# Kernel tuning notes

Hardware: AMD Instinct MI355X
Metric: run time of the kernel (lower is better)

Reference implementation:

```python
import jax, jax.numpy as jnp
import numpy as np

B, T = 64, 50  # batch, decode steps (max_sequence_length)


def setup_inputs() -> dict:
    key = jax.random.key(0)
    ks = jax.random.split(key, 6)
    D, H, V = 512, 1024, 32000
    s = 0.02
    return {
        "sequence_embedding": jax.random.normal(ks[0], (B, H), jnp.float32),
        "emb_table": jax.random.normal(ks[1], (V, D), jnp.float32) * s,
        "W_ih": jax.random.normal(ks[2], (3 * H, D), jnp.float32) * s,
        "W_hh": jax.random.normal(ks[3], (3 * H, H), jnp.float32) * s,
        "b_ih": jnp.zeros((3 * H,), jnp.float32),
        "b_hh": jnp.zeros((3 * H,), jnp.float32),
        "fc_w": jax.random.normal(ks[4], (V, H), jnp.float32) * s,
        "fc_b": jnp.zeros((V,), jnp.float32),
        "eos_index": 0,
    }


def _gru_cell(x, h, W_ih, W_hh, b_ih, b_hh):
    # Standard GRU cell (torch GRUCell math). x: [B, D], h: [B, H]
    gi = x @ W_ih.T + b_ih            # [B, 3H]
    gh = h @ W_hh.T + b_hh            # [B, 3H]
    i_r, i_z, i_n = jnp.split(gi, 3, axis=-1)
    h_r, h_z, h_n = jnp.split(gh, 3, axis=-1)
    r = jax.nn.sigmoid(i_r + h_r)
    z = jax.nn.sigmoid(i_z + h_z)
    n = jnp.tanh(i_n + r * h_n)
    return (1.0 - z) * n + z * h


def reference(sequence_embedding, emb_table, W_ih, W_hh, b_ih, b_hh, fc_w, fc_b, eos_index):
    # Initial input: EOS token embedding broadcast over batch. [B, D]
    x0 = jnp.broadcast_to(emb_table[eos_index], (B, emb_table.shape[1]))
    h0 = sequence_embedding  # num_layers=1: initial hidden = sequence embedding
    keys = jax.random.split(jax.random.key(42), T)

    def step(carry, k):
        x, h = carry
        h = _gru_cell(x, h, W_ih, W_hh, b_ih, b_hh)
        logits = h @ fc_w.T + fc_b              # [B, V]
        idx = jax.random.categorical(k, logits)  # multinomial sample, [B]
        x = emb_table[idx]                       # next-step input embedding
        return (x, h), (idx, logits)

    (_, _), (indices, logits) = jax.lax.scan(step, (x0, h0), keys)
    return indices, logits  # [T, B] int, [T, B, V] float
```

## Files before the change

### kernel.cpp

```cpp
#include <hip/hip_runtime.h>
#include <stdint.h>

#define BB 64
#define DD 512
#define HH 1024
#define VV 32000
#define T_STEPS 50
#define G3 3072
#define NBLK_LOG (VV / 64)

typedef __attribute__((ext_vector_type(8))) short bf16x8;
typedef __attribute__((ext_vector_type(4))) float f32x4;
typedef unsigned long long u64;
typedef unsigned short ushort_t;

__device__ __forceinline__ uint32_t rotl32(uint32_t x, int d) {
  return (x << d) | (x >> (32 - d));
}

__device__ __forceinline__ void threefry2x32(uint32_t k0, uint32_t k1,
                                             uint32_t& x0, uint32_t& x1) {
  uint32_t ks0 = k0, ks1 = k1, ks2 = k0 ^ k1 ^ 0x1BD11BDAu;
  x0 += ks0; x1 += ks1;
#define TF_R(r) { x0 += x1; x1 = rotl32(x1, (r)); x1 ^= x0; }
  TF_R(13) TF_R(15) TF_R(26) TF_R(6)
  x0 += ks1; x1 += ks2 + 1u;
  TF_R(17) TF_R(29) TF_R(16) TF_R(24)
  x0 += ks2; x1 += ks0 + 2u;
  TF_R(13) TF_R(15) TF_R(26) TF_R(6)
  x0 += ks0; x1 += ks1 + 3u;
  TF_R(17) TF_R(29) TF_R(16) TF_R(24)
  x0 += ks1; x1 += ks2 + 4u;
  TF_R(13) TF_R(15) TF_R(26) TF_R(6)
  x0 += ks2; x1 += ks0 + 5u;
#undef TF_R
}

__device__ __forceinline__ uint32_t f2bf(float f) {
  uint32_t u = __float_as_uint(f);
  return (u + 0x7fffu + ((u >> 16) & 1u)) >> 16;
}
__device__ __forceinline__ float bf2f(uint32_t b) { return __uint_as_float(b << 16); }

__device__ __forceinline__ u64 packkey(float v, int c) {
  uint32_t s = __float_as_uint(v);
  uint32_t mo = (s & 0x80000000u) ? ~s : (s | 0x80000000u);
  return ((u64)mo << 32) | (uint32_t)(~(uint32_t)c);
}
__device__ __forceinline__ u64 umax64(u64 a, u64 b) { return a > b ? a : b; }

template<int EPI>
__device__ __forceinline__ void mfma_body(
    ushort_t (*__restrict__ bhS)[40], ushort_t (*__restrict__ blS)[40],
    u64 (*__restrict__ scr)[2],
    const ushort_t* __restrict__ Ahi, const ushort_t* __restrict__ Alo,
    const float* __restrict__ Bw, int K,
    const float* __restrict__ bias,
    float* __restrict__ C, int ldc, int n0,
    u64* __restrict__ partial, int nblk, int bid, int t)
{
  const int tid = threadIdx.x;
  const int lane = tid & 63, w = tid >> 6;
  const int l15 = lane & 15, q = lane >> 4;
  const int rw = (w >> 1) * 32, cw = (w & 1) * 32;

  f32x4 acc[2][2] = {};

  const int srow = tid >> 2;
  const int schunk = (tid & 3) * 8;

  for (int k0 = 0; k0 < K; k0 += 32) {
    const float* bp = Bw + (size_t)(n0 + srow) * K + k0 + schunk;
    float4 v0 = *(const float4*)bp;
    float4 v1 = *(const float4*)(bp + 4);

    bf16x8 ah[2], al[2];
#pragma unroll
    for (int m = 0; m < 2; ++m) {
      const size_t ao = (size_t)(rw + 16 * m + l15) * K + k0 + 8 * q;
      ah[m] = *(const bf16x8*)(Ahi + ao);
      al[m] = *(const bf16x8*)(Alo + ao);
    }

    __syncthreads();
    {
      float f[8] = {v0.x, v0.y, v0.z, v0.w, v1.x, v1.y, v1.z, v1.w};
      uint32_t ph[4], pl[4];
#pragma unroll
      for (int i = 0; i < 4; ++i) {
        float a = f[2 * i], b = f[2 * i + 1];
        uint32_t ha = f2bf(a), hb = f2bf(b);
        float ra = a - bf2f(ha), rb = b - bf2f(hb);
        ph[i] = ha | (hb << 16);
        pl[i] = f2bf(ra) | (f2bf(rb) << 16);
      }
      *(uint4*)&bhS[srow][schunk] = make_uint4(ph[0], ph[1], ph[2], ph[3]);
      *(uint4*)&blS[srow][schunk] = make_uint4(pl[0], pl[1], pl[2], pl[3]);
    }
    __syncthreads();

    bf16x8 bhf[2], blf[2];
#pragma unroll
    for (int n = 0; n < 2; ++n) {
      bhf[n] = *(const bf16x8*)&bhS[cw + 16 * n + l15][8 * q];
      blf[n] = *(const bf16x8*)&blS[cw + 16 * n + l15][8 * q];
    }
#pragma unroll
    for (int m = 0; m < 2; ++m)
#pragma unroll
      for (int n = 0; n < 2; ++n) {
        acc[m][n] = __builtin_amdgcn_mfma_f32_16x16x32_bf16(ah[m], bhf[n], acc[m][n], 0, 0, 0);
        acc[m][n] = __builtin_amdgcn_mfma_f32_16x16x32_bf16(ah[m], blf[n], acc[m][n], 0, 0, 0);
        acc[m][n] = __builtin_amdgcn_mfma_f32_16x16x32_bf16(al[m], bhf[n], acc[m][n], 0, 0, 0);
      }
  }

  if constexpr (EPI == 0) {
#pragma unroll
    for (int m = 0; m < 2; ++m)
#pragma unroll
      for (int n = 0; n < 2; ++n)
#pragma unroll
        for (int r = 0; r < 4; ++r) {
          int row = rw + 16 * m + 4 * q + r;
          int col = n0 + cw + 16 * n + l15;
          C[(size_t)row * ldc + col] = acc[m][n][r];
        }
  } else {
    uint32_t kt0 = 0u, kt1 = (uint32_t)t;
    threefry2x32(0u, 42u, kt0, kt1);

    u64 bk[2][4];
#pragma unroll
    for (int m = 0; m < 2; ++m)
#pragma unroll
      for (int r = 0; r < 4; ++r) bk[m][r] = 0ull;

#pragma unroll
    for (int m = 0; m < 2; ++m)
#pragma unroll
      for (int n = 0; n < 2; ++n)
#pragma unroll
        for (int r = 0; r < 4; ++r) {
          int row = rw + 16 * m + 4 * q + r;
          int col = n0 + cw + 16 * n + l15;
          float val = acc[m][n][r] + bias[col];
          C[(size_t)row * ldc + col] = val;
          uint32_t c0 = 0u, c1 = (uint32_t)(row * VV + col);
          threefry2x32(kt0, kt1, c0, c1);
          uint32_t bits = c0 ^ c1;
          float u = __uint_as_float((bits >> 9) | 0x3f800000u) - 1.0f;
          if (u == 0.0f) u = 1.17549435e-38f;
          float g = -__logf(-__logf(u));
          bk[m][r] = umax64(bk[m][r], packkey(val + g, col));
        }
#pragma unroll
    for (int off = 1; off < 16; off <<= 1)
#pragma unroll
      for (int m = 0; m < 2; ++m)
#pragma unroll
        for (int r = 0; r < 4; ++r)
          bk[m][r] = umax64(bk[m][r], (u64)__shfl_xor((long long)bk[m][r], off, 64));

    if (l15 == 0) {
#pragma unroll
      for (int m = 0; m < 2; ++m)
#pragma unroll
        for (int r = 0; r < 4; ++r)
          scr[rw + 16 * m + 4 * q + r][w & 1] = bk[m][r];
    }
    __syncthreads();
    if (tid < 64) {
      u64 fk = umax64(scr[tid][0], scr[tid][1]);
      partial[(size_t)tid * nblk + bid] = fk;
    }
  }
}

__global__ __launch_bounds__(256) void gates_mfma(
    const ushort_t* __restrict__ xh, const ushort_t* __restrict__ xl,
    const float* __restrict__ Wih,
    const ushort_t* __restrict__ hh, const ushort_t* __restrict__ hl,
    const float* __restrict__ Whh,
    float* __restrict__ gi, float* __restrict__ gh)
{
  __shared__ ushort_t bhS[64][40];
  __shared__ ushort_t blS[64][40];
  __shared__ u64 scr[64][2];
  if (blockIdx.x < G3 / 64)
    mfma_body<0>(bhS, blS, scr, xh, xl, Wih, DD, nullptr, gi, G3,
                 blockIdx.x * 64, nullptr, 0, 0, 0);
  else
    mfma_body<0>(bhS, blS, scr, hh, hl, Whh, HH, nullptr, gh, G3,
                 (blockIdx.x - G3 / 64) * 64, nullptr, 0, 0, 0);
}

__global__ __launch_bounds__(256) void logits_mfma(
    const ushort_t* __restrict__ hh, const ushort_t* __restrict__ hl,
    const float* __restrict__ fcw, const float* __restrict__ fcb,
    float* __restrict__ lg, u64* __restrict__ partial, int t)
{
  __shared__ ushort_t bhS[64][40];
  __shared__ ushort_t blS[64][40];
  __shared__ u64 scr[64][2];
  mfma_body<1>(bhS, blS, scr, hh, hl, fcw, HH, fcb, lg, VV,
               blockIdx.x * 64, partial, NBLK_LOG, blockIdx.x, t);
}

__global__ __launch_bounds__(256) void gru_gate(
    const float* __restrict__ gi, const float* __restrict__ gh,
    const float* __restrict__ bih, const float* __restrict__ bhh,
    float* __restrict__ h, ushort_t* __restrict__ hhi, ushort_t* __restrict__ hlo)
{
  int i = blockIdx.x * 256 + threadIdx.x;
  int b = i >> 10, j = i & 1023;
  const float* gib = gi + (size_t)b * G3;
  const float* ghb = gh + (size_t)b * G3;
  float ir = gib[j]        + bih[j],        hr = ghb[j]        + bhh[j];
  float iz = gib[j + 1024] + bih[j + 1024], hz = ghb[j + 1024] + bhh[j + 1024];
  float in_ = gib[j + 2048] + bih[j + 2048], hn = ghb[j + 2048] + bhh[j + 2048];
  float r = 1.f / (1.f + expf(-(ir + hr)));
  float z = 1.f / (1.f + expf(-(iz + hz)));
  float n = tanhf(in_ + r * hn);
  float hv = (1.f - z) * n + z * h[i];
  h[i] = hv;
  uint32_t hb = f2bf(hv);
  hhi[i] = (ushort_t)hb;
  hlo[i] = (ushort_t)f2bf(hv - bf2f(hb));
}

__global__ __launch_bounds__(256) void finish_sample(
    const u64* __restrict__ partial, const float* __restrict__ emb,
    float* __restrict__ idx_out, ushort_t* __restrict__ xh, ushort_t* __restrict__ xl)
{
  __shared__ u64 red[256];
  __shared__ int sidx;
  const int b = blockIdx.x, tid = threadIdx.x;
  u64 best = 0;
  for (int i = tid; i < NBLK_LOG; i += 256) {
    u64 v = partial[(size_t)b * NBLK_LOG + i];
    if (v > best) best = v;
  }
  red[tid] = best;
  __syncthreads();
  for (int s = 128; s > 0; s >>= 1) {
    if (tid < s) { if (red[tid + s] > red[tid]) red[tid] = red[tid + s]; }
    __syncthreads();
  }
  if (tid == 0) {
    int idx = (int)(~(uint32_t)red[0]);
    sidx = idx;
    idx_out[b] = (float)idx;
  }
  __syncthreads();
  const float2* ep = (const float2*)(emb + (size_t)sidx * DD);
  float2 v = ep[tid];
  uint32_t h0 = f2bf(v.x), h1 = f2bf(v.y);
  uint32_t l0 = f2bf(v.x - bf2f(h0)), l1 = f2bf(v.y - bf2f(h1));
  *(uint32_t*)&xh[(size_t)b * DD + 2 * tid] = h0 | (h1 << 16);
  *(uint32_t*)&xl[(size_t)b * DD + 2 * tid] = l0 | (l1 << 16);
}

__global__ __launch_bounds__(256) void init_kernel(
    const float* __restrict__ seq, const float* __restrict__ emb,
    const int* __restrict__ eos, float* __restrict__ h,
    ushort_t* __restrict__ hhi, ushort_t* __restrict__ hlo,
    ushort_t* __restrict__ xh, ushort_t* __restrict__ xl)
{
  int i = blockIdx.x * 256 + threadIdx.x;
  if (i < BB * HH) {
    float v = seq[i];
    h[i] = v;
    uint32_t hb = f2bf(v);
    hhi[i] = (ushort_t)hb;
    hlo[i] = (ushort_t)f2bf(v - bf2f(hb));
  }
  if (i < BB * DD) {
    float v = emb[(size_t)eos[0] * DD + (i & (DD - 1))];
    uint32_t hb = f2bf(v);
    xh[i] = (ushort_t)hb;
    xl[i] = (ushort_t)f2bf(v - bf2f(hb));
  }
}

extern "C" void kernel_launch(void* const* d_in, const int* in_sizes, int n_in,
                              void* d_out, int out_size, void* d_ws, size_t ws_size,
                              hipStream_t stream) {
  const float* seq = (const float*)d_in[0];
  const float* emb = (const float*)d_in[1];
  const float* Wih = (const float*)d_in[2];
  const float* Whh = (const float*)d_in[3];
  const float* bih = (const float*)d_in[4];
  const float* bhh = (const float*)d_in[5];
  const float* fcw = (const float*)d_in[6];
  const float* fcb = (const float*)d_in[7];
  const int*   eos = (const int*)d_in[8];

  float* out = (float*)d_out;
  float* idx_out = out;
  float* log_out = out + (size_t)T_STEPS * BB;

  uint8_t* wsp = (uint8_t*)d_ws;
  auto alloc = [&](size_t bytes) {
    uint8_t* p = wsp;
    wsp += (bytes + 255) & ~(size_t)255;
    return p;
  };
  float*    h    = (float*)alloc((size_t)BB * HH * 4);
  float*    gi   = (float*)alloc((size_t)BB * G3 * 4);
  float*    gh   = (float*)alloc((size_t)BB * G3 * 4);
  ushort_t* hhi  = (ushort_t*)alloc((size_t)BB * HH * 2);
  ushort_t* hlo  = (ushort_t*)alloc((size_t)BB * HH * 2);
  ushort_t* xh   = (ushort_t*)alloc((size_t)BB * DD * 2);
  ushort_t* xl   = (ushort_t*)alloc((size_t)BB * DD * 2);
  u64*      part = (u64*)alloc((size_t)BB * NBLK_LOG * 8);

  init_kernel<<<256, 256, 0, stream>>>(seq, emb, eos, h, hhi, hlo, xh, xl);

  for (int t = 0; t < T_STEPS; ++t) {
    float* lg = log_out + (size_t)t * BB * VV;
    gates_mfma<<<96, 256, 0, stream>>>(xh, xl, Wih, hhi, hlo, Whh, gi, gh);
    gru_gate<<<(BB * HH) / 256, 256, 0, stream>>>(gi, gh, bih, bhh, h, hhi, hlo);
    logits_mfma<<<NBLK_LOG, 256, 0, stream>>>(hhi, hlo, fcw, fcb, lg, part, t);
    finish_sample<<<BB, 256, 0, stream>>>(part, emb, idx_out + t * BB, xh, xl);
  }
}
```

Baseline: 3.830 ms.

## Fuse decoder into persistent cooperative kernel with precomputed embedding-input projections

After: 8.579 ms. 124% more time.

```diff
diff --git a/kernel.cpp b/kernel.cpp
--- a/kernel.cpp
+++ b/kernel.cpp
@@ -1,5 +1,8 @@
 #include <hip/hip_runtime.h>
+#include <hip/hip_cooperative_groups.h>
 #include <stdint.h>
+
+namespace cg = cooperative_groups;
 
 #define BB 64
 #define DD 512
@@ -7,7 +10,9 @@
 #define VV 32000
 #define T_STEPS 50
 #define G3 3072
-#define NBLK_LOG (VV / 64)
+#define NT 250
+#define GHT 24
+#define UT 12000
 
 typedef __attribute__((ext_vector_type(8))) short bf16x8;
 typedef __attribute__((ext_vector_type(4))) float f32x4;
@@ -49,25 +54,34 @@
 }
 __device__ __forceinline__ u64 umax64(u64 a, u64 b) { return a > b ? a : b; }
 
-template<int EPI>
-__device__ __forceinline__ void mfma_body(
+union BF8 { uint32_t u[4]; bf16x8 v; };
+
+__device__ __forceinline__ void split8(const float* f, bf16x8& hi, bf16x8& lo) {
+  BF8 H, L;
+#pragma unroll
+  for (int i = 0; i < 4; ++i) {
+    float a = f[2 * i], b = f[2 * i + 1];
+    uint32_t ha = f2bf(a), hb = f2bf(b);
+    float ra = a - bf2f(ha), rb = b - bf2f(hb);
+    H.u[i] = ha | (hb << 16);
+    L.u[i] = f2bf(ra) | (f2bf(rb) << 16);
+  }
+  hi = H.v; lo = L.v;
+}
+
+template<bool AF32>
+__device__ __forceinline__ void mfma_tile512(
     ushort_t (*__restrict__ bhS)[40], ushort_t (*__restrict__ blS)[40],
-    u64 (*__restrict__ scr)[2],
     const ushort_t* __restrict__ Ahi, const ushort_t* __restrict__ Alo,
-    const float* __restrict__ Bw, int K,
-    const float* __restrict__ bias,
-    float* __restrict__ C, int ldc, int n0,
-    u64* __restrict__ partial, int nblk, int bid, int t)
+    const float* __restrict__ Af, int lda,
+    const float* __restrict__ Bw, int K, int n0,
+    f32x4 acc[2][2])
 {
   const int tid = threadIdx.x;
   const int lane = tid & 63, w = tid >> 6;
   const int l15 = lane & 15, q = lane >> 4;
-  const int rw = (w >> 1) * 32, cw = (w & 1) * 32;
-
-  f32x4 acc[2][2] = {};
-
-  const int srow = tid >> 2;
-  const int schunk = (tid & 3) * 8;
+  const int rw = (w >> 2) * 32, cw = (w & 3) * 32;
+  const int srow = tid >> 2, schunk = (tid & 3) * 8;
 
   for (int k0 = 0; k0 < K; k0 += 32) {
     const float* bp = Bw + (size_t)(n0 + srow) * K + k0 + schunk;
@@ -77,25 +91,26 @@
     bf16x8 ah[2], al[2];
 #pragma unroll
     for (int m = 0; m < 2; ++m) {
-      const size_t ao = (size_t)(rw + 16 * m + l15) * K + k0 + 8 * q;
-      ah[m] = *(const bf16x8*)(Ahi + ao);
-      al[m] = *(const bf16x8*)(Alo + ao);
+      if constexpr (AF32) {
+        const float* ap = Af + (size_t)(rw + 16 * m + l15) * lda + k0 + 8 * q;
+        float4 a0 = *(const float4*)ap;
+        float4 a1 = *(const float4*)(ap + 4);
+        float f[8] = {a0.x, a0.y, a0.z, a0.w, a1.x, a1.y, a1.z, a1.w};
+        split8(f, ah[m], al[m]);
+      } else {
+        const size_t ao = (size_t)(rw + 16 * m + l15) * lda + k0 + 8 * q;
+        ah[m] = *(const bf16x8*)(Ahi + ao);
+        al[m] = *(const bf16x8*)(Alo + ao);
+      }
     }
 
     __syncthreads();
     {
       float f[8] = {v0.x, v0.y, v0.z, v0.w, v1.x, v1.y, v1.z, v1.w};
-      uint32_t ph[4], pl[4];
-#pragma unroll
-      for (int i = 0; i < 4; ++i) {
-        float a = f[2 * i], b = f[2 * i + 1];
-        uint32_t ha = f2bf(a), hb = f2bf(b);
-        float ra = a - bf2f(ha), rb = b - bf2f(hb);
-        ph[i] = ha | (hb << 16);
-        pl[i] = f2bf(ra) | (f2bf(rb) << 16);
-      }
-      *(uint4*)&bhS[srow][schunk] = make_uint4(ph[0], ph[1], ph[2], ph[3]);
-      *(uint4*)&blS[srow][schunk] = make_uint4(pl[0], pl[1], pl[2], pl[3]);
+      bf16x8 bh, bl;
+      split8(f, bh, bl);
+      *(bf16x8*)&bhS[srow][schunk] = bh;
+      *(bf16x8*)&blS[srow][schunk] = bl;
     }
     __syncthreads();
 
@@ -114,111 +129,108 @@
         acc[m][n] = __builtin_amdgcn_mfma_f32_16x16x32_bf16(al[m], bhf[n], acc[m][n], 0, 0, 0);
       }
   }
-
-  if constexpr (EPI == 0) {
+}
+
+__device__ __forceinline__ void store_tile512(f32x4 acc[2][2], float* __restrict__ C,
+                                              int ldc, int n0)
+{
+  const int tid = threadIdx.x, lane = tid & 63, w = tid >> 6;
+  const int l15 = lane & 15, q = lane >> 4;
+  const int rw = (w >> 2) * 32, cw = (w & 3) * 32;
+#pragma unroll
+  for (int m = 0; m < 2; ++m)
+#pragma unroll
+    for (int n = 0; n < 2; ++n)
+#pragma unroll
+      for (int r = 0; r < 4; ++r)
+        C[(size_t)(rw + 16 * m + 4 * q + r) * ldc + n0 + cw + 16 * n + l15] = acc[m][n][r];
+}
+
+__device__ __forceinline__ void sample_epi512(
+    f32x4 acc[2][2], u64 (*__restrict__ scr)[4],
+    const float* __restrict__ bias, float* __restrict__ C, int n0,
+    u64* __restrict__ partial, int jobid, int t)
+{
+  const int tid = threadIdx.x, lane = tid & 63, w = tid >> 6;
+  const int l15 = lane & 15, q = lane >> 4;
+  const int rw = (w >> 2) * 32, cw = (w & 3) * 32;
+
+  uint32_t kt0 = 0u, kt1 = (uint32_t)t;
+  threefry2x32(0u, 42u, kt0, kt1);
+
+  u64 bk[2][4];
+#pragma unroll
+  for (int m = 0; m < 2; ++m)
+#pragma unroll
+    for (int r = 0; r < 4; ++r) bk[m][r] = 0ull;
+
+#pragma unroll
+  for (int m = 0; m < 2; ++m)
+#pragma unroll
+    for (int n = 0; n < 2; ++n)
+#pragma unroll
+      for (int r = 0; r < 4; ++r) {
+        int row = rw + 16 * m + 4 * q + r;
+        int col = n0 + cw + 16 * n + l15;
+        float val = acc[m][n][r] + bias[col];
+        C[(size_t)row * VV + col] = val;
+        uint32_t c0 = 0u, c1 = (uint32_t)(row * VV + col);
+        threefry2x32(kt0, kt1, c0, c1);
+        uint32_t bits = c0 ^ c1;
+        float u = __uint_as_float((bits >> 9) | 0x3f800000u) - 1.0f;
+        if (u == 0.0f) u = 1.17549435e-38f;
+        float g = -__logf(-__logf(u));
+        bk[m][r] = umax64(bk[m][r], packkey(val + g, col));
+      }
+#pragma unroll
+  for (int off = 1; off < 16; off <<= 1)
 #pragma unroll
     for (int m = 0; m < 2; ++m)
 #pragma unroll
-      for (int n = 0; n < 2; ++n)
-#pragma unroll
-        for (int r = 0; r < 4; ++r) {
-          int row = rw + 16 * m + 4 * q + r;
-          int col = n0 + cw + 16 * n + l15;
-          C[(size_t)row * ldc + col] = acc[m][n][r];
-        }
-  } else {
-    uint32_t kt0 = 0u, kt1 = (uint32_t)t;
-    threefry2x32(0u, 42u, kt0, kt1);
-
-    u64 bk[2][4];
+      for (int r = 0; r < 4; ++r)
+        bk[m][r] = umax64(bk[m][r], (u64)__shfl_xor((long long)bk[m][r], off, 64));
+
+  if (l15 == 0) {
 #pragma unroll
     for (int m = 0; m < 2; ++m)
 #pragma unroll
-      for (int r = 0; r < 4; ++r) bk[m][r] = 0ull;
-
-#pragma unroll
-    for (int m = 0; m < 2; ++m)
-#pragma unroll
-      for (int n = 0; n < 2; ++n)
-#pragma unroll
-        for (int r = 0; r < 4; ++r) {
-          int row = rw + 16 * m + 4 * q + r;
-          int col = n0 + cw + 16 * n + l15;
-          float val = acc[m][n][r] + bias[col];
-          C[(size_t)row * ldc + col] = val;
-          uint32_t c0 = 0u, c1 = (uint32_t)(row * VV + col);
-          threefry2x32(kt0, kt1, c0, c1);
-          uint32_t bits = c0 ^ c1;
-          float u = __uint_as_float((bits >> 9) | 0x3f800000u) - 1.0f;
-          if (u == 0.0f) u = 1.17549435e-38f;
-          float g = -__logf(-__logf(u));
-          bk[m][r] = umax64(bk[m][r], packkey(val + g, col));
-        }
-#pragma unroll
-    for (int off = 1; off < 16; off <<= 1)
-#pragma unroll
-      for (int m = 0; m < 2; ++m)
-#pragma unroll
-        for (int r = 0; r < 4; ++r)
-          bk[m][r] = umax64(bk[m][r], (u64)__shfl_xor((long long)bk[m][r], off, 64));
-
-    if (l15 == 0) {
-#pragma unroll
-      for (int m = 0; m < 2; ++m)
-#pragma unroll
-        for (int r = 0; r < 4; ++r)
-          scr[rw + 16 * m + 4 * q + r][w & 1] = bk[m][r];
-    }
+      for (int r = 0; r < 4; ++r)
+        scr[rw + 16 * m + 4 * q + r][w & 3] = bk[m][r];
+  }
+  __syncthreads();
+  if (tid < 64) {
+    u64 f = umax64(umax64(scr[tid][0], scr[tid][1]),
+                   umax64(scr[tid][2], scr[tid][3]));
+    partial[(size_t)tid * NT + jobid] = f;
+  }
+  __syncthreads();
+}
+
+__device__ __forceinline__ int finish_reduce(const u64* __restrict__ partial,
+                                             int b, u64* __restrict__ sred)
+{
+  const int tid = threadIdx.x;
+  u64 best = 0;
+  if (tid < NT) best = partial[(size_t)b * NT + tid];
+  sred[tid] = best;
+  __syncthreads();
+  for (int s = 256; s > 0; s >>= 1) {
+    if (tid < s) sred[tid] = umax64(sred[tid], sred[tid + s]);
     __syncthreads();
-    if (tid < 64) {
-      u64 fk = umax64(scr[tid][0], scr[tid][1]);
-      partial[(size_t)tid * nblk + bid] = fk;
-    }
-  }
-}
-
-__global__ __launch_bounds__(256) void gates_mfma(
-    const ushort_t* __restrict__ xh, const ushort_t* __restrict__ xl,
-    const float* __restrict__ Wih,
-    const ushort_t* __restrict__ hh, const ushort_t* __restrict__ hl,
-    const float* __restrict__ Whh,
-    float* __restrict__ gi, float* __restrict__ gh)
-{
-  __shared__ ushort_t bhS[64][40];
-  __shared__ ushort_t blS[64][40];
-  __shared__ u64 scr[64][2];
-  if (blockIdx.x < G3 / 64)
-    mfma_body<0>(bhS, blS, scr, xh, xl, Wih, DD, nullptr, gi, G3,
-                 blockIdx.x * 64, nullptr, 0, 0, 0);
-  else
-    mfma_body<0>(bhS, blS, scr, hh, hl, Whh, HH, nullptr, gh, G3,
-                 (blockIdx.x - G3 / 64) * 64, nullptr, 0, 0, 0);
-}
-
-__global__ __launch_bounds__(256) void logits_mfma(
-    const ushort_t* __restrict__ hh, const ushort_t* __restrict__ hl,
-    const float* __restrict__ fcw, const float* __restrict__ fcb,
-    float* __restrict__ lg, u64* __restrict__ partial, int t)
-{
-  __shared__ ushort_t bhS[64][40];
-  __shared__ ushort_t blS[64][40];
-  __shared__ u64 scr[64][2];
-  mfma_body<1>(bhS, blS, scr, hh, hl, fcw, HH, fcb, lg, VV,
-               blockIdx.x * 64, partial, NBLK_LOG, blockIdx.x, t);
-}
-
-__global__ __launch_bounds__(256) void gru_gate(
-    const float* __restrict__ gi, const float* __restrict__ gh,
+  }
+  return (int)(~(uint32_t)sred[0]);
+}
+
+__device__ __forceinline__ void fuse_elem(
+    const float* __restrict__ gir, const float* __restrict__ ghr,
     const float* __restrict__ bih, const float* __restrict__ bhh,
-    float* __restrict__ h, ushort_t* __restrict__ hhi, ushort_t* __restrict__ hlo)
-{
-  int i = blockIdx.x * 256 + threadIdx.x;
-  int b = i >> 10, j = i & 1023;
-  const float* gib = gi + (size_t)b * G3;
-  const float* ghb = gh + (size_t)b * G3;
-  float ir = gib[j]        + bih[j],        hr = ghb[j]        + bhh[j];
-  float iz = gib[j + 1024] + bih[j + 1024], hz = ghb[j + 1024] + bhh[j + 1024];
-  float in_ = gib[j + 2048] + bih[j + 2048], hn = ghb[j + 2048] + bhh[j + 2048];
+    float* __restrict__ h, ushort_t* __restrict__ hhi, ushort_t* __restrict__ hlo,
+    int b, int j)
+{
+  int i = b * HH + j;
+  float ir  = gir[j]        + bih[j],        hr = ghr[j]        + bhh[j];
+  float iz  = gir[j + 1024] + bih[j + 1024], hz = ghr[j + 1024] + bhh[j + 1024];
+  float in_ = gir[j + 2048] + bih[j + 2048], hn = ghr[j + 2048] + bhh[j + 2048];
   float r = 1.f / (1.f + expf(-(ir + hr)));
   float z = 1.f / (1.f + expf(-(iz + hz)));
   float n = tanhf(in_ + r * hn);
@@ -229,58 +241,204 @@
   hlo[i] = (ushort_t)f2bf(hv - bf2f(hb));
 }
 
-__global__ __launch_bounds__(256) void finish_sample(
-    const u64* __restrict__ partial, const float* __restrict__ emb,
-    float* __restrict__ idx_out, ushort_t* __restrict__ xh, ushort_t* __restrict__ xl)
-{
-  __shared__ u64 red[256];
-  __shared__ int sidx;
-  const int b = blockIdx.x, tid = threadIdx.x;
-  u64 best = 0;
-  for (int i = tid; i < NBLK_LOG; i += 256) {
-    u64 v = partial[(size_t)b * NBLK_LOG + i];
-    if (v > best) best = v;
-  }
-  red[tid] = best;
-  __syncthreads();
-  for (int s = 128; s > 0; s >>= 1) {
-    if (tid < s) { if (red[tid + s] > red[tid]) red[tid] = red[tid + s]; }
-    __syncthreads();
-  }
-  if (tid == 0) {
-    int idx = (int)(~(uint32_t)red[0]);
-    sidx = idx;
-    idx_out[b] = (float)idx;
-  }
-  __syncthreads();
-  const float2* ep = (const float2*)(emb + (size_t)sidx * DD);
-  float2 v = ep[tid];
-  uint32_t h0 = f2bf(v.x), h1 = f2bf(v.y);
-  uint32_t l0 = f2bf(v.x - bf2f(h0)), l1 = f2bf(v.y - bf2f(h1));
-  *(uint32_t*)&xh[(size_t)b * DD + 2 * tid] = h0 | (h1 << 16);
-  *(uint32_t*)&xl[(size_t)b * DD + 2 * tid] = l0 | (l1 << 16);
-}
-
-__global__ __launch_bounds__(256) void init_kernel(
+template<bool USE_U>
+__global__ __launch_bounds__(512, 2) void decoder_all(
     const float* __restrict__ seq, const float* __restrict__ emb,
-    const int* __restrict__ eos, float* __restrict__ h,
+    const float* __restrict__ Wih, const float* __restrict__ Whh,
+    const float* __restrict__ bih, const float* __restrict__ bhh,
+    const float* __restrict__ fcw, const float* __restrict__ fcb,
+    const int* __restrict__ eos,
+    float* __restrict__ idx_out, float* __restrict__ log_out,
+    float* __restrict__ U, float* __restrict__ h,
     ushort_t* __restrict__ hhi, ushort_t* __restrict__ hlo,
-    ushort_t* __restrict__ xh, ushort_t* __restrict__ xl)
-{
-  int i = blockIdx.x * 256 + threadIdx.x;
-  if (i < BB * HH) {
+    float* __restrict__ gh, float* __restrict__ gi,
+    ushort_t* __restrict__ xh, ushort_t* __restrict__ xl,
+    u64* __restrict__ partial)
+{
+  cg::grid_group grid = cg::this_grid();
+  __shared__ ushort_t bhS[128][40];
+  __shared__ ushort_t blS[128][40];
+  __shared__ u64 scr[64][4];
+  __shared__ u64 sred[512];
+  const int bid = blockIdx.x, tid = threadIdx.x;
+  const int GRD = gridDim.x;
+  const int eosv = eos[0];
+
+  for (int i = bid * 512 + tid; i < BB * HH; i += GRD * 512) {
     float v = seq[i];
     h[i] = v;
     uint32_t hb = f2bf(v);
     hhi[i] = (ushort_t)hb;
     hlo[i] = (ushort_t)f2bf(v - bf2f(hb));
   }
-  if (i < BB * DD) {
-    float v = emb[(size_t)eos[0] * DD + (i & (DD - 1))];
+  if constexpr (!USE_U) {
+    for (int i = bid * 512 + tid; i < BB * DD; i += GRD * 512) {
+      float v = emb[(size_t)eosv * DD + (i & (DD - 1))];
+      uint32_t hb = f2bf(v);
+      xh[i] = (ushort_t)hb;
+      xl[i] = (ushort_t)f2bf(v - bf2f(hb));
+    }
+  }
+  grid.sync();
+  if constexpr (USE_U) {
+    for (int tile = bid; tile < UT + GHT; tile += GRD) {
+      f32x4 acc[2][2] = {};
+      if (tile < UT) {
+        int r0 = (tile / 24) * 64, c0 = (tile % 24) * 128;
+        mfma_tile512<true>(bhS, blS, nullptr, nullptr, emb + (size_t)r0 * DD, DD,
+                           Wih, DD, c0, acc);
+        store_tile512(acc, U + (size_t)r0 * G3, G3, c0);
+      } else {
+        int g = tile - UT;
+        mfma_tile512<false>(bhS, blS, hhi, hlo, nullptr, HH, Whh, HH, g * 128, acc);
+        store_tile512(acc, gh, G3, g * 128);
+      }
+    }
+  }
+  grid.sync();
+
+  for (int t = 0; t <= T_STEPS; ++t) {
+    for (int i0 = bid * 512; i0 < BB * HH; i0 += GRD * 512) {
+      const int b = i0 >> 10, half = (i0 >> 9) & 1;
+      int idx;
+      if (t == 0) idx = eosv;
+      else idx = finish_reduce(partial, b, sred);
+      if (t > 0 && half == 0 && tid == 0)
+        idx_out[(size_t)(t - 1) * BB + b] = (float)idx;
+      if (t < T_STEPS) {
+        if constexpr (USE_U) {
+          const int j = (half << 9) + tid;
+          fuse_elem(U + (size_t)idx * G3, gh + (size_t)b * G3, bih, bhh,
+                    h, hhi, hlo, b, j);
+        } else {
+          if (half == 0) {
+            float v = emb[(size_t)idx * DD + tid];
+            uint32_t hb = f2bf(v);
+            xh[(size_t)b * DD + tid] = (ushort_t)hb;
+            xl[(size_t)b * DD + tid] = (ushort_t)f2bf(v - bf2f(hb));
+          }
+        }
+      }
+    }
+    if (t == T_STEPS) break;
+    grid.sync();
+
+    if constexpr (!USE_U) {
+      for (int job = bid; job < 2 * GHT; job += GRD) {
+        f32x4 acc[2][2] = {};
+        if (job < GHT) {
+          mfma_tile512<false>(bhS, blS, xh, xl, nullptr, DD, Wih, DD, job * 128, acc);
+          store_tile512(acc, gi, G3, job * 128);
+        } else {
+          int g = job - GHT;
+          mfma_tile512<false>(bhS, blS, hhi, hlo, nullptr, HH, Whh, HH, g * 128, acc);
+          store_tile512(acc, gh, G3, g * 128);
+        }
+      }
+      grid.sync();
+      for (int i0 = bid * 512; i0 < BB * HH; i0 += GRD * 512) {
+        const int b = i0 >> 10, half = (i0 >> 9) & 1;
+        const int j = (half << 9) + tid;
+        fuse_elem(gi + (size_t)b * G3, gh + (size_t)b * G3, bih, bhh,
+                  h, hhi, hlo, b, j);
+      }
+      grid.sync();
+    }
+
+    const int NJ = USE_U ? (NT + GHT) : NT;
+    for (int job = bid; job < NJ; job += GRD) {
+      f32x4 acc[2][2] = {};
+      if (job < NT) {
+        mfma_tile512<false>(bhS, blS, hhi, hlo, nullptr, HH, fcw, HH, job * 128, acc);
+        sample_epi512(acc, scr, fcb, log_out + (size_t)t * BB * VV, job * 128,
+                      partial, job, t);
+      } else {
+        int g = job - NT;
+        mfma_tile512<false>(bhS, blS, hhi, hlo, nullptr, HH, Whh, HH, g * 128, acc);
+        store_tile512(acc, gh, G3, g * 128);
+      }
+    }
+    grid.sync();
+  }
+}
+
+__global__ __launch_bounds__(512) void k_init(
+    const float* __restrict__ seq, const float* __restrict__ emb,
+    const int* __restrict__ eos, float* __restrict__ h,
+    ushort_t* __restrict__ hhi, ushort_t* __restrict__ hlo,
+    ushort_t* __restrict__ xh, ushort_t* __restrict__ xl)
+{
+  const int eosv = eos[0];
+  for (int i = blockIdx.x * 512 + threadIdx.x; i < BB * HH; i += gridDim.x * 512) {
+    float v = seq[i];
+    h[i] = v;
+    uint32_t hb = f2bf(v);
+    hhi[i] = (ushort_t)hb;
+    hlo[i] = (ushort_t)f2bf(v - bf2f(hb));
+  }
+  for (int i = blockIdx.x * 512 + threadIdx.x; i < BB * DD; i += gridDim.x * 512) {
+    float v = emb[(size_t)eosv * DD + (i & (DD - 1))];
     uint32_t hb = f2bf(v);
     xh[i] = (ushort_t)hb;
     xl[i] = (ushort_t)f2bf(v - bf2f(hb));
   }
+}
+
+__global__ __launch_bounds__(512, 2) void k_gates(
+    const ushort_t* __restrict__ xh, const ushort_t* __restrict__ xl,
+    const ushort_t* __restrict__ hhi, const ushort_t* __restrict__ hlo,
+    const float* __restrict__ Wih, const float* __restrict__ Whh,
+    float* __restrict__ gi, float* __restrict__ gh)
+{
+  __shared__ ushort_t bhS[128][40];
+  __shared__ ushort_t blS[128][40];
+  int job = blockIdx.x;
+  f32x4 acc[2][2] = {};
+  if (job < GHT) {
+    mfma_tile512<false>(bhS, blS, xh, xl, nullptr, DD, Wih, DD, job * 128, acc);
+    store_tile512(acc, gi, G3, job * 128);
+  } else {
+    int g = job - GHT;
+    mfma_tile512<false>(bhS, blS, hhi, hlo, nullptr, HH, Whh, HH, g * 128, acc);
+    store_tile512(acc, gh, G3, g * 128);
+  }
+}
+
+__global__ __launch_bounds__(512) void k_fuse(
+    const float* __restrict__ gi, const float* __restrict__ gh,
+    const float* __restrict__ bih, const float* __restrict__ bhh,
+    float* __restrict__ h, ushort_t* __restrict__ hhi, ushort_t* __restrict__ hlo)
+{
+  int i = blockIdx.x * 512 + threadIdx.x;
+  int b = i >> 10, j = i & 1023;
+  fuse_elem(gi + (size_t)b * G3, gh + (size_t)b * G3, bih, bhh, h, hhi, hlo, b, j);
+}
+
+__global__ __launch_bounds__(512, 2) void k_logits(
+    const ushort_t* __restrict__ hhi, const ushort_t* __restrict__ hlo,
+    const float* __restrict__ fcw, const float* __restrict__ fcb,
+    float* __restrict__ lg, u64* __restrict__ partial, int t)
+{
+  __shared__ ushort_t bhS[128][40];
+  __shared__ ushort_t blS[128][40];
+  __shared__ u64 scr[64][4];
+  f32x4 acc[2][2] = {};
+  mfma_tile512<false>(bhS, blS, hhi, hlo, nullptr, HH, fcw, HH, blockIdx.x * 128, acc);
+  sample_epi512(acc, scr, fcb, lg, blockIdx.x * 128, partial, blockIdx.x, t);
+}
+
+__global__ __launch_bounds__(512) void k_finish(
+    const u64* __restrict__ partial, const float* __restrict__ emb,
+    float* __restrict__ idx_t, ushort_t* __restrict__ xh, ushort_t* __restrict__ xl)
+{
+  __shared__ u64 sred[512];
+  const int b = blockIdx.x, tid = threadIdx.x;
+  int idx = finish_reduce(partial, b, sred);
+  if (tid == 0) idx_t[b] = (float)idx;
+  float v = emb[(size_t)idx * DD + tid];
+  uint32_t hb = f2bf(v);
+  xh[(size_t)b * DD + tid] = (ushort_t)hb;
+  xl[(size_t)b * DD + tid] = (ushort_t)f2bf(v - bf2f(hb));
 }
 
 extern "C" void kernel_launch(void* const* d_in, const int* in_sizes, int n_in,
@@ -307,21 +465,46 @@
     return p;
   };
   float*    h    = (float*)alloc((size_t)BB * HH * 4);
-  float*    gi   = (float*)alloc((size_t)BB * G3 * 4);
-  float*    gh   = (float*)alloc((size_t)BB * G3 * 4);
   ushort_t* hhi  = (ushort_t*)alloc((size_t)BB * HH * 2);
   ushort_t* hlo  = (ushort_t*)alloc((size_t)BB * HH * 2);
+  float*    gh   = (float*)alloc((size_t)BB * G3 * 4);
+  float*    gi   = (float*)alloc((size_t)BB * G3 * 4);
   ushort_t* xh   = (ushort_t*)alloc((size_t)BB * DD * 2);
   ushort_t* xl   = (ushort_t*)alloc((size_t)BB * DD * 2);
-  u64*      part = (u64*)alloc((size_t)BB * NBLK_LOG * 8);
-
-  init_kernel<<<256, 256, 0, stream>>>(seq, emb, eos, h, hhi, hlo, xh, xl);
-
-  for (int t = 0; t < T_STEPS; ++t) {
-    float* lg = log_out + (size_t)t * BB * VV;
-    gates_mfma<<<96, 256, 0, stream>>>(xh, xl, Wih, hhi, hlo, Whh, gi, gh);
-    gru_gate<<<(BB * HH) / 256, 256, 0, stream>>>(gi, gh, bih, bhh, h, hhi, hlo);
-    logits_mfma<<<NBLK_LOG, 256, 0, stream>>>(hhi, hlo, fcw, fcb, lg, part, t);
-    finish_sample<<<BB, 256, 0, stream>>>(part, emb, idx_out + t * BB, xh, xl);
-  }
-}
+  u64*      part = (u64*)alloc((size_t)BB * NT * 8);
+  float*    U    = (float*)alloc((size_t)VV * G3 * 4);
+
+  size_t need_u = (size_t)((uint8_t*)wsp - (uint8_t*)d_ws);
+  bool useU = need_u <= ws_size;
+
+  const void* kfn = useU ? reinterpret_cast<const void*>(&decoder_all<true>)
+                         : reinterpret_cast<const void*>(&decoder_all<false>);
+
+  int dev = 0;
+  (void)hipGetDevice(&dev);
+  int numCU = 0;
+  (void)hipDeviceGetAttribute(&numCU, hipDeviceAttributeMultiprocessorCount, dev);
+  int occ = 0;
+  hipError_t qe = hipOccupancyMaxActiveBlocksPerMultiprocessor(&occ, kfn, 512, 0);
+  long grid = (qe == hipSuccess && numCU > 0) ? (long)occ * (long)numCU : 0;
+  if (grid > 512) grid = 512;
+
+  hipError_t err = hipErrorUnknown;
+  if (grid >= 64) {
+    void* args[] = {&seq, &emb, &Wih, &Whh, &bih, &bhh, &fcw, &fcb, &eos,
+                    &idx_out, &log_out, &U, &h, &hhi, &hlo, &gh, &gi,
+                    &xh, &xl, &part};
+    err = hipLaunchCooperativeKernel(kfn, dim3((uint32_t)grid), dim3(512),
+                                     args, 0, stream);
+  }
+  if (err != hipSuccess) {
+    k_init<<<128, 512, 0, stream>>>(seq, emb, eos, h, hhi, hlo, xh, xl);
+    for (int t = 0; t < T_STEPS; ++t) {
+      float* lg = log_out + (size_t)t * BB * VV;
+      k_gates<<<2 * GHT, 512, 0, stream>>>(xh, xl, hhi, hlo, Wih, Whh, gi, gh);
+      k_fuse<<<128, 512, 0, stream>>>(gi, gh, bih, bhh, h, hhi, hlo);
+      k_logits<<<NT, 512, 0, stream>>>(hhi, hlo, fcw, fcb, lg, part, t);
+      k_finish<<<BB, 512, 0, stream>>>(part, emb, idx_out + (size_t)t * BB, xh, xl);
+    }
+  }
+}
```
